# Performance work log

Measured on AMD Instinct MI355X. Metric: run time of the kernel, lower is better.

The kernel has to match this reference:

```python
import jax, jax.numpy as jnp
import numpy as np

H = 1024        # hidden_size
E = 8           # num_experts
K = 2           # top_k
FF = 4 * H      # expert hidden dim
B, S = 2, 2048


def setup_inputs() -> dict:
    key = jax.random.key(0)
    ks = jax.random.split(key, 7)
    scale = 0.02
    x = jax.random.normal(ks[0], (B, S, H), dtype=jnp.float32)
    Wg = jax.random.normal(ks[1], (H, E), dtype=jnp.float32) * scale
    bg = jnp.zeros((E,), dtype=jnp.float32)
    W1 = jax.random.normal(ks[2], (E, H, FF), dtype=jnp.float32) * scale
    b1 = jnp.zeros((E, FF), dtype=jnp.float32)
    W2 = jax.random.normal(ks[3], (E, FF, H), dtype=jnp.float32) * scale
    b2 = jnp.zeros((E, H), dtype=jnp.float32)
    return {"x": x, "Wg": Wg, "bg": bg, "W1": W1, "b1": b1, "W2": W2, "b2": b2}


def reference(x, Wg, bg, W1, b1, W2, b2):
    b, s, h = x.shape
    xf = x.reshape(-1, h)                                  # [T, H]
    T = xf.shape[0]
    # gating: softmax -> top-k -> renormalize
    probs = jax.nn.softmax(xf @ Wg + bg, axis=-1)          # [T, E]
    vals, idx = jax.lax.top_k(probs, K)                    # [T, K]
    vals = vals / jnp.sum(vals, axis=-1, keepdims=True)
    # dense combine weights: zero for non-selected experts (equivalent math)
    combine = jnp.zeros((T, E), dtype=x.dtype)
    combine = combine.at[jnp.arange(T)[:, None], idx].set(vals)  # [T, E]
    # all-expert FFN (GEMM-dominated), combined with sparse gate weights
    hmid = jax.nn.gelu(jnp.einsum('th,ehf->tef', xf, W1) + b1, approximate=False)  # [T,E,FF]
    y = jnp.einsum('tef,efh->teh', hmid, W2) + b2          # [T, E, H]
    out = jnp.einsum('te,teh->th', combine, y)             # [T, H]
    return out.reshape(b, s, h)
```

## Files before the change

kernel.cpp:

```cpp
#include <hip/hip_runtime.h>
#include <hip/hip_bf16.h>
#include <math.h>

#define T_TOK  4096
#define H_DIM  1024
#define E_NUM  8
#define FF_DIM 4096
#define KSEL   2
#define SLOTS  (T_TOK*KSEL)
#define SLOTS_PAD (SLOTS + 256)
#define BM 128
#define MAXTILES 72

typedef __attribute__((ext_vector_type(8))) short s16x8;
typedef __attribute__((ext_vector_type(8))) unsigned short u16x8;
typedef __attribute__((ext_vector_type(4))) float f32x4;

typedef __attribute__((address_space(1))) const void global_cvoid;
typedef __attribute__((address_space(3))) void lds_void;

__device__ __forceinline__ unsigned short f2bf(float f){
  unsigned int u = __float_as_uint(f);
  u += 0x7fffu + ((u>>16)&1u);
  return (unsigned short)(u>>16);
}
__device__ __forceinline__ float bf2f(unsigned short h){
  return __uint_as_float(((unsigned int)h)<<16);
}

static constexpr size_t OFF_CNT   = 0;
static constexpr size_t OFF_OFFS  = 256;
static constexpr size_t OFF_NT    = 512;
static constexpr size_t OFF_TILES = 768;
static constexpr size_t OFF_IDX   = 1280;
static constexpr size_t OFF_POS   = OFF_IDX  + 32768;
static constexpr size_t OFF_WV    = OFF_POS  + 32768;
static constexpr size_t OFF_SLOT  = OFF_WV   + 32768;
static constexpr size_t OFF_TOK   = OFF_SLOT + 32768;
static constexpr size_t OFF_WOF   = OFF_TOK  + 32768;
static constexpr size_t OFF_XG    = OFF_WOF  + 32768;
static constexpr size_t OFF_W1T   = OFF_XG  + (size_t)SLOTS_PAD*H_DIM*2;
static constexpr size_t OFF_W2T   = OFF_W1T + (size_t)E_NUM*H_DIM*FF_DIM*2;
static constexpr size_t OFF_MID   = OFF_W2T + (size_t)E_NUM*H_DIM*FF_DIM*2;
static constexpr size_t OFF_Y     = OFF_MID + (size_t)SLOTS_PAD*FF_DIM*2;

__global__ __launch_bounds__(64) void gate_kernel(
    const float* __restrict__ x, const float* __restrict__ Wg,
    const float* __restrict__ bg, int* __restrict__ cnt,
    int* __restrict__ idxp, int* __restrict__ posp, float* __restrict__ wvp)
{
  int t = blockIdx.x, lane = threadIdx.x;
  const float* xr = x + (size_t)t*H_DIM;
  float acc[E_NUM];
  #pragma unroll
  for (int e=0;e<E_NUM;e++) acc[e]=0.f;
  for (int i=0;i<H_DIM/64;i++){
    int h = i*64 + lane;
    float xv = xr[h];
    const float* wr_ = Wg + (size_t)h*E_NUM;
    #pragma unroll
    for (int e=0;e<E_NUM;e++) acc[e] += xv*wr_[e];
  }
  #pragma unroll
  for (int e=0;e<E_NUM;e++){
    #pragma unroll
    for (int off=32; off>0; off>>=1) acc[e] += __shfl_xor(acc[e], off);
  }
  if (lane==0){
    float l[E_NUM];
    #pragma unroll
    for (int e=0;e<E_NUM;e++) l[e] = acc[e] + bg[e];
    int i0 = 0;
    #pragma unroll
    for (int e=1;e<E_NUM;e++) if (l[e] > l[i0]) i0 = e;
    int i1 = (i0==0)?1:0;
    #pragma unroll
    for (int e=0;e<E_NUM;e++) if (e!=i0 && l[e] > l[i1]) i1 = e;
    float p1 = expf(l[i1]-l[i0]);
    float s  = 1.f + p1;
    float w0 = 1.f/s, w1 = p1/s;
    int pos0 = atomicAdd(&cnt[i0],1);
    int pos1 = atomicAdd(&cnt[i1],1);
    idxp[t*2]=i0; idxp[t*2+1]=i1;
    posp[t*2]=pos0; posp[t*2+1]=pos1;
    wvp[t*2]=w0; wvp[t*2+1]=w1;
  }
}

__global__ void plan_kernel(const int* __restrict__ cnt, int* __restrict__ offs,
                            int* __restrict__ tiles, int* __restrict__ ntiles)
{
  int o=0, n=0;
  for (int e=0;e<E_NUM;e++){
    offs[e]=o;
    int c=cnt[e];
    int nt=(c+BM-1)/BM;
    for (int m=0;m<nt;m++) tiles[n++] = (e<<16)|m;
    o+=c;
  }
  offs[E_NUM]=o;
  *ntiles=n;
}

__global__ void scatter_kernel(const int* __restrict__ idxp, const int* __restrict__ posp,
                               const float* __restrict__ wvp, const int* __restrict__ offs,
                               int* __restrict__ tok_of, float* __restrict__ w_of,
                               int* __restrict__ slot_of)
{
  int i = blockIdx.x*blockDim.x + threadIdx.x;
  if (i >= SLOTS) return;
  int t = i>>1, k = i&1;
  int e = idxp[t*2+k];
  int slot = offs[e] + posp[t*2+k];
  tok_of[slot] = t;
  w_of[slot]   = wvp[t*2+k];
  slot_of[t*2+k] = slot;
}

__global__ __launch_bounds__(256) void gather_kernel(
    const float* __restrict__ x, const int* __restrict__ tok_of,
    unsigned short* __restrict__ Xg)
{
  int slot = blockIdx.x;
  int t = tok_of[slot];
  const float4* src = (const float4*)(x + (size_t)t*H_DIM);
  float4 v = src[threadIdx.x];
  ushort4 o;
  o.x=f2bf(v.x); o.y=f2bf(v.y); o.z=f2bf(v.z); o.w=f2bf(v.w);
  ((ushort4*)(Xg + (size_t)slot*H_DIM))[threadIdx.x] = o;
}

__global__ __launch_bounds__(256) void transconv_kernel(
    const float* __restrict__ in, unsigned short* __restrict__ out, int R, int C)
{
  __shared__ float tile[64][65];
  int e = blockIdx.z;
  const float* inp = in + (size_t)e*R*C;
  unsigned short* op = out + (size_t)e*R*C;
  int c0 = blockIdx.x*64, r0 = blockIdx.y*64;
  int tx = threadIdx.x & 15, ty = threadIdx.x >> 4;
  #pragma unroll
  for (int i=0;i<4;i++){
    int r = i*16 + ty;
    float4 v = *(const float4*)(inp + (size_t)(r0+r)*C + c0 + tx*4);
    tile[r][tx*4+0]=v.x; tile[r][tx*4+1]=v.y; tile[r][tx*4+2]=v.z; tile[r][tx*4+3]=v.w;
  }
  __syncthreads();
  int wx = threadIdx.x & 7;
  int wcl = threadIdx.x >> 3;
  #pragma unroll
  for (int i=0;i<2;i++){
    int c = i*32 + wcl;
    u16x8 o;
    #pragma unroll
    for (int j=0;j<8;j++) o[j] = f2bf(tile[wx*8+j][c]);
    *(u16x8*)(op + (size_t)(c0+c)*R + r0 + wx*8) = o;
  }
}

#define GLDS(g, l) __builtin_amdgcn_global_load_lds((global_cvoid*)(g), (lds_void*)(l), 16, 0, 0)

template<int MODE>
__global__ __launch_bounds__(256, 4) void gemm128_kernel(
    const unsigned short* __restrict__ A,
    const unsigned short* __restrict__ Bt,
    const float* __restrict__ bias,
    unsigned short* __restrict__ Out,
    const int* __restrict__ tiles, const int* __restrict__ ntiles,
    const int* __restrict__ cnt, const int* __restrict__ offs,
    const float* __restrict__ w_of,
    int N, int K, int cshift)
{
  int tile_id = blockIdx.x >> cshift;
  if (tile_id >= *ntiles) return;
  int col0 = (blockIdx.x & ((1<<cshift)-1)) << 7;
  int packed = tiles[tile_id];
  int e = packed>>16, mt = packed & 0xffff;
  int row0 = offs[e] + mt*BM;
  int nvalid = cnt[e] - mt*BM; if (nvalid > BM) nvalid = BM;
  const unsigned short* Be = Bt + (size_t)e*N*K;

  __shared__ unsigned short As[2][128*32];
  __shared__ unsigned short Bs[2][128*32];
  char* asb = (char*)&As[0][0];
  char* bsb = (char*)&Bs[0][0];

  int t = threadIdx.x;
  int wid = t>>6, lane = t&63;
  int wr = (wid>>1)*64, wc = (wid&1)*64;
  int fr = lane&15, fq = lane>>4;

  int srow = t>>2;
  int sclog = ((t&3) - ((t>>3)&3)) & 3;
  int sdst = wid*1024;

  const unsigned short* gA0 = A  + (size_t)(row0 + srow)*K      + sclog*8;
  const unsigned short* gA1 = A  + (size_t)(row0 + 64 + srow)*K + sclog*8;
  const unsigned short* gB0 = Be + (size_t)(col0 + srow)*K      + sclog*8;
  const unsigned short* gB1 = Be + (size_t)(col0 + 64 + srow)*K + sclog*8;

  auto stage = [&](int buf, int kelem){
    GLDS(gA0 + kelem, asb + buf*8192 + sdst);
    GLDS(gA1 + kelem, asb + buf*8192 + 4096 + sdst);
    GLDS(gB0 + kelem, bsb + buf*8192 + sdst);
    GLDS(gB1 + kelem, bsb + buf*8192 + 4096 + sdst);
  };

  int rd_sw = ((fq + ((fr>>1)&3)) & 3) << 4;

  f32x4 acc[4][4];
  #pragma unroll
  for (int i=0;i<4;i++)
    #pragma unroll
    for (int j=0;j<4;j++) acc[i][j] = (f32x4){0.f,0.f,0.f,0.f};

  int NT = K >> 5;
  stage(0, 0);
  stage(1, 32);
  for (int kt=0; kt<NT; ++kt){
    int cur = kt&1;
    if (kt+1 < NT) asm volatile("s_waitcnt vmcnt(4)" ::: "memory");
    else           asm volatile("s_waitcnt vmcnt(0)" ::: "memory");
    __builtin_amdgcn_s_barrier();
    asm volatile("" ::: "memory");

    s16x8 af[4], bfr[4];
    #pragma unroll
    for (int i=0;i<4;i++){
      af[i]  = *(const s16x8*)(asb + cur*8192 + (wr + i*16 + fr)*64 + rd_sw);
      bfr[i] = *(const s16x8*)(bsb + cur*8192 + (wc + i*16 + fr)*64 + rd_sw);
    }
    #pragma unroll
    for (int i=0;i<4;i++)
      #pragma unroll
      for (int j=0;j<4;j++)
        acc[i][j] = __builtin_amdgcn_mfma_f32_16x16x32_bf16(af[i], bfr[j], acc[i][j], 0,0,0);

    asm volatile("s_waitcnt lgkmcnt(0)" ::: "memory");
    __builtin_amdgcn_s_barrier();
    asm volatile("" ::: "memory");
    if (kt+2 < NT) stage(cur, (kt+2)*32);
  }

  #pragma unroll
  for (int i=0;i<4;i++){
    #pragma unroll
    for (int r=0;r<4;r++){
      int lrow = wr + i*16 + fq*4 + r;
      if (lrow < nvalid){
        int grow = row0 + lrow;
        float scale = (MODE==1) ? w_of[grow] : 0.f;
        #pragma unroll
        for (int j=0;j<4;j++){
          int col = col0 + wc + j*16 + fr;
          float v = acc[i][j][r] + bias[(size_t)e*N + col];
          if (MODE==0) v = 0.5f*v*(1.f + erff(v*0.70710678118654752f));
          else         v *= scale;
          Out[(size_t)grow*N + col] = f2bf(v);
        }
      }
    }
  }
}

__global__ __launch_bounds__(256) void combine_kernel(
    const unsigned short* __restrict__ y, const int* __restrict__ slot_of,
    float* __restrict__ out)
{
  int tok = blockIdx.x;
  int s0 = slot_of[tok*2], s1 = slot_of[tok*2+1];
  const ushort4* y0 = (const ushort4*)(y + (size_t)s0*H_DIM);
  const ushort4* y1 = (const ushort4*)(y + (size_t)s1*H_DIM);
  float4* o = (float4*)(out + (size_t)tok*H_DIM);
  ushort4 a = y0[threadIdx.x], b = y1[threadIdx.x];
  float4 r;
  r.x = bf2f(a.x)+bf2f(b.x);
  r.y = bf2f(a.y)+bf2f(b.y);
  r.z = bf2f(a.z)+bf2f(b.z);
  r.w = bf2f(a.w)+bf2f(b.w);
  o[threadIdx.x] = r;
}

extern "C" void kernel_launch(void* const* d_in, const int* in_sizes, int n_in,
                              void* d_out, int out_size, void* d_ws, size_t ws_size,
                              hipStream_t stream) {
  const float* x  = (const float*)d_in[0];
  const float* Wg = (const float*)d_in[1];
  const float* bg = (const float*)d_in[2];
  const float* W1 = (const float*)d_in[3];
  const float* b1 = (const float*)d_in[4];
  const float* W2 = (const float*)d_in[5];
  const float* b2 = (const float*)d_in[6];
  float* out = (float*)d_out;
  char* ws = (char*)d_ws;

  int*   cnt      = (int*)  (ws + OFF_CNT);
  int*   offs     = (int*)  (ws + OFF_OFFS);
  int*   ntiles   = (int*)  (ws + OFF_NT);
  int*   tiles    = (int*)  (ws + OFF_TILES);
  int*   idxp     = (int*)  (ws + OFF_IDX);
  int*   posp     = (int*)  (ws + OFF_POS);
  float* wvp      = (float*)(ws + OFF_WV);
  int*   slot_of  = (int*)  (ws + OFF_SLOT);
  int*   tok_of   = (int*)  (ws + OFF_TOK);
  float* w_of     = (float*)(ws + OFF_WOF);
  unsigned short* Xg  = (unsigned short*)(ws + OFF_XG);
  unsigned short* W1t = (unsigned short*)(ws + OFF_W1T);
  unsigned short* W2t = (unsigned short*)(ws + OFF_W2T);
  unsigned short* mid = (unsigned short*)(ws + OFF_MID);
  unsigned short* y   = (unsigned short*)(ws + OFF_Y);

  hipMemsetAsync(ws + OFF_CNT, 0, 32, stream);

  gate_kernel<<<T_TOK, 64, 0, stream>>>(x, Wg, bg, cnt, idxp, posp, wvp);
  plan_kernel<<<1, 1, 0, stream>>>(cnt, offs, tiles, ntiles);
  scatter_kernel<<<SLOTS/256, 256, 0, stream>>>(idxp, posp, wvp, offs, tok_of, w_of, slot_of);
  gather_kernel<<<SLOTS, 256, 0, stream>>>(x, tok_of, Xg);

  transconv_kernel<<<dim3(FF_DIM/64, H_DIM/64, E_NUM), 256, 0, stream>>>(W1, W1t, H_DIM, FF_DIM);
  transconv_kernel<<<dim3(H_DIM/64, FF_DIM/64, E_NUM), 256, 0, stream>>>(W2, W2t, FF_DIM, H_DIM);

  gemm128_kernel<0><<<dim3(MAXTILES*32), 256, 0, stream>>>(
      Xg, W1t, b1, mid, tiles, ntiles, cnt, offs, nullptr, FF_DIM, H_DIM, 5);
  gemm128_kernel<1><<<dim3(MAXTILES*8), 256, 0, stream>>>(
      mid, W2t, b2, y, tiles, ntiles, cnt, offs, w_of, H_DIM, FF_DIM, 3);

  combine_kernel<<<T_TOK, 256, 0, stream>>>(y, slot_of, out);
}
```

Before: 463.5 us.

## Use 2-wave GEMM tiles and fuse combine into second GEMM via atomics

Rewrites the expert GEMM to run 128-thread blocks where each of two waves computes a 64x128 slice, so each wave does more MFMAs per B-fragment load. The second GEMM now scales by the gate weight and atomically adds fp32 results straight into the output, which removes the bf16 y buffer and the separate combine kernel. The output is zeroed with a memset. The gate kernel also handles four tokens per block. Risks are fewer waves to hide latency, higher register pressure from the 4x8 accumulators, and contention from the fp32 atomics.

```diff
diff --git a/kernel.cpp b/kernel.cpp
--- a/kernel.cpp
+++ b/kernel.cpp
@@ -35,55 +35,56 @@
 static constexpr size_t OFF_IDX   = 1280;
 static constexpr size_t OFF_POS   = OFF_IDX  + 32768;
 static constexpr size_t OFF_WV    = OFF_POS  + 32768;
-static constexpr size_t OFF_SLOT  = OFF_WV   + 32768;
-static constexpr size_t OFF_TOK   = OFF_SLOT + 32768;
+static constexpr size_t OFF_TOK   = OFF_WV   + 32768;
 static constexpr size_t OFF_WOF   = OFF_TOK  + 32768;
 static constexpr size_t OFF_XG    = OFF_WOF  + 32768;
 static constexpr size_t OFF_W1T   = OFF_XG  + (size_t)SLOTS_PAD*H_DIM*2;
 static constexpr size_t OFF_W2T   = OFF_W1T + (size_t)E_NUM*H_DIM*FF_DIM*2;
 static constexpr size_t OFF_MID   = OFF_W2T + (size_t)E_NUM*H_DIM*FF_DIM*2;
-static constexpr size_t OFF_Y     = OFF_MID + (size_t)SLOTS_PAD*FF_DIM*2;
 
 __global__ __launch_bounds__(64) void gate_kernel(
     const float* __restrict__ x, const float* __restrict__ Wg,
     const float* __restrict__ bg, int* __restrict__ cnt,
     int* __restrict__ idxp, int* __restrict__ posp, float* __restrict__ wvp)
 {
-  int t = blockIdx.x, lane = threadIdx.x;
-  const float* xr = x + (size_t)t*H_DIM;
-  float acc[E_NUM];
-  #pragma unroll
-  for (int e=0;e<E_NUM;e++) acc[e]=0.f;
-  for (int i=0;i<H_DIM/64;i++){
-    int h = i*64 + lane;
-    float xv = xr[h];
-    const float* wr_ = Wg + (size_t)h*E_NUM;
-    #pragma unroll
-    for (int e=0;e<E_NUM;e++) acc[e] += xv*wr_[e];
-  }
-  #pragma unroll
-  for (int e=0;e<E_NUM;e++){
-    #pragma unroll
-    for (int off=32; off>0; off>>=1) acc[e] += __shfl_xor(acc[e], off);
-  }
-  if (lane==0){
-    float l[E_NUM];
-    #pragma unroll
-    for (int e=0;e<E_NUM;e++) l[e] = acc[e] + bg[e];
-    int i0 = 0;
-    #pragma unroll
-    for (int e=1;e<E_NUM;e++) if (l[e] > l[i0]) i0 = e;
-    int i1 = (i0==0)?1:0;
-    #pragma unroll
-    for (int e=0;e<E_NUM;e++) if (e!=i0 && l[e] > l[i1]) i1 = e;
-    float p1 = expf(l[i1]-l[i0]);
-    float s  = 1.f + p1;
-    float w0 = 1.f/s, w1 = p1/s;
-    int pos0 = atomicAdd(&cnt[i0],1);
-    int pos1 = atomicAdd(&cnt[i1],1);
-    idxp[t*2]=i0; idxp[t*2+1]=i1;
-    posp[t*2]=pos0; posp[t*2+1]=pos1;
-    wvp[t*2]=w0; wvp[t*2+1]=w1;
+  int lane = threadIdx.x;
+  for (int tt=0; tt<4; ++tt){
+    int t = blockIdx.x*4 + tt;
+    const float* xr = x + (size_t)t*H_DIM;
+    float acc[E_NUM];
+    #pragma unroll
+    for (int e=0;e<E_NUM;e++) acc[e]=0.f;
+    for (int i=0;i<H_DIM/64;i++){
+      int h = i*64 + lane;
+      float xv = xr[h];
+      const float* wr_ = Wg + (size_t)h*E_NUM;
+      #pragma unroll
+      for (int e=0;e<E_NUM;e++) acc[e] += xv*wr_[e];
+    }
+    #pragma unroll
+    for (int e=0;e<E_NUM;e++){
+      #pragma unroll
+      for (int off=32; off>0; off>>=1) acc[e] += __shfl_xor(acc[e], off);
+    }
+    if (lane==0){
+      float l[E_NUM];
+      #pragma unroll
+      for (int e=0;e<E_NUM;e++) l[e] = acc[e] + bg[e];
+      int i0 = 0;
+      #pragma unroll
+      for (int e=1;e<E_NUM;e++) if (l[e] > l[i0]) i0 = e;
+      int i1 = (i0==0)?1:0;
+      #pragma unroll
+      for (int e=0;e<E_NUM;e++) if (e!=i0 && l[e] > l[i1]) i1 = e;
+      float p1 = expf(l[i1]-l[i0]);
+      float s  = 1.f + p1;
+      float w0 = 1.f/s, w1 = p1/s;
+      int pos0 = atomicAdd(&cnt[i0],1);
+      int pos1 = atomicAdd(&cnt[i1],1);
+      idxp[t*2]=i0; idxp[t*2+1]=i1;
+      posp[t*2]=pos0; posp[t*2+1]=pos1;
+      wvp[t*2]=w0; wvp[t*2+1]=w1;
+    }
   }
 }
 
@@ -104,8 +105,7 @@
 
 __global__ void scatter_kernel(const int* __restrict__ idxp, const int* __restrict__ posp,
                                const float* __restrict__ wvp, const int* __restrict__ offs,
-                               int* __restrict__ tok_of, float* __restrict__ w_of,
-                               int* __restrict__ slot_of)
+                               int* __restrict__ tok_of, float* __restrict__ w_of)
 {
   int i = blockIdx.x*blockDim.x + threadIdx.x;
   if (i >= SLOTS) return;
@@ -114,7 +114,6 @@
   int slot = offs[e] + posp[t*2+k];
   tok_of[slot] = t;
   w_of[slot]   = wvp[t*2+k];
-  slot_of[t*2+k] = slot;
 }
 
 __global__ __launch_bounds__(256) void gather_kernel(
@@ -161,11 +160,13 @@
 #define GLDS(g, l) __builtin_amdgcn_global_load_lds((global_cvoid*)(g), (lds_void*)(l), 16, 0, 0)
 
 template<int MODE>
-__global__ __launch_bounds__(256, 4) void gemm128_kernel(
+__global__ __launch_bounds__(128, 2) void gemm128w2_kernel(
     const unsigned short* __restrict__ A,
     const unsigned short* __restrict__ Bt,
     const float* __restrict__ bias,
     unsigned short* __restrict__ Out,
+    float* __restrict__ OutF,
+    const int* __restrict__ tok_of,
     const int* __restrict__ tiles, const int* __restrict__ ntiles,
     const int* __restrict__ cnt, const int* __restrict__ offs,
     const float* __restrict__ w_of,
@@ -180,61 +181,56 @@
   int nvalid = cnt[e] - mt*BM; if (nvalid > BM) nvalid = BM;
   const unsigned short* Be = Bt + (size_t)e*N*K;
 
-  __shared__ unsigned short As[2][128*32];
-  __shared__ unsigned short Bs[2][128*32];
-  char* asb = (char*)&As[0][0];
-  char* bsb = (char*)&Bs[0][0];
+  __shared__ char asb[2*8192];
+  __shared__ char bsb[2*8192];
 
   int t = threadIdx.x;
-  int wid = t>>6, lane = t&63;
-  int wr = (wid>>1)*64, wc = (wid&1)*64;
+  int w = t>>6, lane = t&63;
   int fr = lane&15, fq = lane>>4;
 
-  int srow = t>>2;
-  int sclog = ((t&3) - ((t>>3)&3)) & 3;
-  int sdst = wid*1024;
-
-  const unsigned short* gA0 = A  + (size_t)(row0 + srow)*K      + sclog*8;
-  const unsigned short* gA1 = A  + (size_t)(row0 + 64 + srow)*K + sclog*8;
-  const unsigned short* gB0 = Be + (size_t)(col0 + srow)*K      + sclog*8;
-  const unsigned short* gB1 = Be + (size_t)(col0 + 64 + srow)*K + sclog*8;
+  int srow = lane>>2;
+  int scl  = ((lane&3) - ((lane>>3)&3)) & 3;
+  const unsigned short* pA = A  + (size_t)(row0 + w*64 + srow)*K + scl*8;
+  const unsigned short* pB = Be + (size_t)(col0 + w*64 + srow)*K + scl*8;
 
   auto stage = [&](int buf, int kelem){
-    GLDS(gA0 + kelem, asb + buf*8192 + sdst);
-    GLDS(gA1 + kelem, asb + buf*8192 + 4096 + sdst);
-    GLDS(gB0 + kelem, bsb + buf*8192 + sdst);
-    GLDS(gB1 + kelem, bsb + buf*8192 + 4096 + sdst);
+    #pragma unroll
+    for (int i=0;i<4;i++){
+      GLDS(pA + (size_t)i*16*K + kelem, asb + buf*8192 + w*4096 + i*1024);
+      GLDS(pB + (size_t)i*16*K + kelem, bsb + buf*8192 + w*4096 + i*1024);
+    }
   };
 
-  int rd_sw = ((fq + ((fr>>1)&3)) & 3) << 4;
-
-  f32x4 acc[4][4];
+  int rdc = ((fq + ((fr>>1)&3)) & 3) << 4;
+
+  f32x4 acc[4][8];
   #pragma unroll
-  for (int i=0;i<4;i++)
-    #pragma unroll
-    for (int j=0;j<4;j++) acc[i][j] = (f32x4){0.f,0.f,0.f,0.f};
+  for (int m=0;m<4;m++)
+    #pragma unroll
+    for (int n=0;n<8;n++) acc[m][n] = (f32x4){0.f,0.f,0.f,0.f};
 
   int NT = K >> 5;
   stage(0, 0);
   stage(1, 32);
   for (int kt=0; kt<NT; ++kt){
     int cur = kt&1;
-    if (kt+1 < NT) asm volatile("s_waitcnt vmcnt(4)" ::: "memory");
+    if (kt+1 < NT) asm volatile("s_waitcnt vmcnt(8)" ::: "memory");
     else           asm volatile("s_waitcnt vmcnt(0)" ::: "memory");
     __builtin_amdgcn_s_barrier();
     asm volatile("" ::: "memory");
 
-    s16x8 af[4], bfr[4];
-    #pragma unroll
-    for (int i=0;i<4;i++){
-      af[i]  = *(const s16x8*)(asb + cur*8192 + (wr + i*16 + fr)*64 + rd_sw);
-      bfr[i] = *(const s16x8*)(bsb + cur*8192 + (wc + i*16 + fr)*64 + rd_sw);
-    }
-    #pragma unroll
-    for (int i=0;i<4;i++)
-      #pragma unroll
-      for (int j=0;j<4;j++)
-        acc[i][j] = __builtin_amdgcn_mfma_f32_16x16x32_bf16(af[i], bfr[j], acc[i][j], 0,0,0);
+    s16x8 af[4], bfr[8];
+    #pragma unroll
+    for (int m=0;m<4;m++)
+      af[m] = *(const s16x8*)(asb + cur*8192 + (w*64 + m*16 + fr)*64 + rdc);
+    #pragma unroll
+    for (int n=0;n<8;n++)
+      bfr[n] = *(const s16x8*)(bsb + cur*8192 + (n*16 + fr)*64 + rdc);
+    #pragma unroll
+    for (int m=0;m<4;m++)
+      #pragma unroll
+      for (int n=0;n<8;n++)
+        acc[m][n] = __builtin_amdgcn_mfma_f32_16x16x32_bf16(af[m], bfr[n], acc[m][n], 0,0,0);
 
     asm volatile("s_waitcnt lgkmcnt(0)" ::: "memory");
     __builtin_amdgcn_s_barrier();
@@ -243,42 +239,33 @@
   }
 
   #pragma unroll
-  for (int i=0;i<4;i++){
+  for (int m=0;m<4;m++){
     #pragma unroll
     for (int r=0;r<4;r++){
-      int lrow = wr + i*16 + fq*4 + r;
+      int lrow = w*64 + m*16 + fq*4 + r;
       if (lrow < nvalid){
         int grow = row0 + lrow;
-        float scale = (MODE==1) ? w_of[grow] : 0.f;
-        #pragma unroll
-        for (int j=0;j<4;j++){
-          int col = col0 + wc + j*16 + fr;
-          float v = acc[i][j][r] + bias[(size_t)e*N + col];
-          if (MODE==0) v = 0.5f*v*(1.f + erff(v*0.70710678118654752f));
-          else         v *= scale;
-          Out[(size_t)grow*N + col] = f2bf(v);
+        if (MODE==0){
+          #pragma unroll
+          for (int n=0;n<8;n++){
+            int col = col0 + n*16 + fr;
+            float v = acc[m][n][r] + bias[(size_t)e*N + col];
+            v = 0.5f*v*(1.f + erff(v*0.70710678118654752f));
+            Out[(size_t)grow*N + col] = f2bf(v);
+          }
+        } else {
+          int tok = tok_of[grow];
+          float scale = w_of[grow];
+          #pragma unroll
+          for (int n=0;n<8;n++){
+            int col = col0 + n*16 + fr;
+            float v = (acc[m][n][r] + bias[(size_t)e*N + col]) * scale;
+            atomicAdd(&OutF[(size_t)tok*H_DIM + col], v);
+          }
         }
       }
     }
   }
-}
-
-__global__ __launch_bounds__(256) void combine_kernel(
-    const unsigned short* __restrict__ y, const int* __restrict__ slot_of,
-    float* __restrict__ out)
-{
-  int tok = blockIdx.x;
-  int s0 = slot_of[tok*2], s1 = slot_of[tok*2+1];
-  const ushort4* y0 = (const ushort4*)(y + (size_t)s0*H_DIM);
-  const ushort4* y1 = (const ushort4*)(y + (size_t)s1*H_DIM);
-  float4* o = (float4*)(out + (size_t)tok*H_DIM);
-  ushort4 a = y0[threadIdx.x], b = y1[threadIdx.x];
-  float4 r;
-  r.x = bf2f(a.x)+bf2f(b.x);
-  r.y = bf2f(a.y)+bf2f(b.y);
-  r.z = bf2f(a.z)+bf2f(b.z);
-  r.w = bf2f(a.w)+bf2f(b.w);
-  o[threadIdx.x] = r;
 }
 
 extern "C" void kernel_launch(void* const* d_in, const int* in_sizes, int n_in,
@@ -301,29 +288,28 @@
   int*   idxp     = (int*)  (ws + OFF_IDX);
   int*   posp     = (int*)  (ws + OFF_POS);
   float* wvp      = (float*)(ws + OFF_WV);
-  int*   slot_of  = (int*)  (ws + OFF_SLOT);
   int*   tok_of   = (int*)  (ws + OFF_TOK);
   float* w_of     = (float*)(ws + OFF_WOF);
   unsigned short* Xg  = (unsigned short*)(ws + OFF_XG);
   unsigned short* W1t = (unsigned short*)(ws + OFF_W1T);
   unsigned short* W2t = (unsigned short*)(ws + OFF_W2T);
   unsigned short* mid = (unsigned short*)(ws + OFF_MID);
-  unsigned short* y   = (unsigned short*)(ws + OFF_Y);
 
   hipMemsetAsync(ws + OFF_CNT, 0, 32, stream);
-
-  gate_kernel<<<T_TOK, 64, 0, stream>>>(x, Wg, bg, cnt, idxp, posp, wvp);
+  hipMemsetAsync(d_out, 0, (size_t)out_size*sizeof(float), stream);
+
+  gate_kernel<<<T_TOK/4, 64, 0, stream>>>(x, Wg, bg, cnt, idxp, posp, wvp);
   plan_kernel<<<1, 1, 0, stream>>>(cnt, offs, tiles, ntiles);
-  scatter_kernel<<<SLOTS/256, 256, 0, stream>>>(idxp, posp, wvp, offs, tok_of, w_of, slot_of);
+  scatter_kernel<<<SLOTS/256, 256, 0, stream>>>(idxp, posp, wvp, offs, tok_of, w_of);
   gather_kernel<<<SLOTS, 256, 0, stream>>>(x, tok_of, Xg);
 
   transconv_kernel<<<dim3(FF_DIM/64, H_DIM/64, E_NUM), 256, 0, stream>>>(W1, W1t, H_DIM, FF_DIM);
   transconv_kernel<<<dim3(H_DIM/64, FF_DIM/64, E_NUM), 256, 0, stream>>>(W2, W2t, FF_DIM, H_DIM);
 
-  gemm128_kernel<0><<<dim3(MAXTILES*32), 256, 0, stream>>>(
-      Xg, W1t, b1, mid, tiles, ntiles, cnt, offs, nullptr, FF_DIM, H_DIM, 5);
-  gemm128_kernel<1><<<dim3(MAXTILES*8), 256, 0, stream>>>(
-      mid, W2t, b2, y, tiles, ntiles, cnt, offs, w_of, H_DIM, FF_DIM, 3);
-
-  combine_kernel<<<T_TOK, 256, 0, stream>>>(y, slot_of, out);
-}
+  gemm128w2_kernel<0><<<dim3(MAXTILES*32), 128, 0, stream>>>(
+      Xg, W1t, b1, mid, nullptr, tok_of, tiles, ntiles, cnt, offs, nullptr,
+      FF_DIM, H_DIM, 5);
+  gemm128w2_kernel<1><<<dim3(MAXTILES*8), 128, 0, stream>>>(
+      mid, W2t, b2, nullptr, out, tok_of, tiles, ntiles, cnt, offs, w_of,
+      H_DIM, FF_DIM, 3);
+}
```

Result: slower. 571.0 us (+23.2%).

## Use 256x256 tiled GEMM for first expert FFN layer with new tile plan

Applied to the files above, without the earlier changes.

Adds a 512-thread gemm256s kernel with 256x256 output tiles, K-step 64, XOR-swizzled LDS and double buffering for the first expert GEMM. The plan kernel now also builds a 256-row tile list, so each block reuses more of A and B per load. The gate kernel now processes four tokens per block to cut launch count. The bigger tiles waste more work on padded rows per expert, and occupancy falls to two blocks of 128 KB LDS each.

```diff
diff --git a/kernel.cpp b/kernel.cpp
--- a/kernel.cpp
+++ b/kernel.cpp
@@ -11,6 +11,7 @@
 #define SLOTS_PAD (SLOTS + 256)
 #define BM 128
 #define MAXTILES 72
+#define MAXT256  40
 
 typedef __attribute__((ext_vector_type(8))) short s16x8;
 typedef __attribute__((ext_vector_type(8))) unsigned short u16x8;
@@ -31,7 +32,9 @@
 static constexpr size_t OFF_CNT   = 0;
 static constexpr size_t OFF_OFFS  = 256;
 static constexpr size_t OFF_NT    = 512;
+static constexpr size_t OFF_NT256 = 516;
 static constexpr size_t OFF_TILES = 768;
+static constexpr size_t OFF_T256  = 1088;
 static constexpr size_t OFF_IDX   = 1280;
 static constexpr size_t OFF_POS   = OFF_IDX  + 32768;
 static constexpr size_t OFF_WV    = OFF_POS  + 32768;
@@ -49,57 +52,64 @@
     const float* __restrict__ bg, int* __restrict__ cnt,
     int* __restrict__ idxp, int* __restrict__ posp, float* __restrict__ wvp)
 {
-  int t = blockIdx.x, lane = threadIdx.x;
-  const float* xr = x + (size_t)t*H_DIM;
-  float acc[E_NUM];
-  #pragma unroll
-  for (int e=0;e<E_NUM;e++) acc[e]=0.f;
-  for (int i=0;i<H_DIM/64;i++){
-    int h = i*64 + lane;
-    float xv = xr[h];
-    const float* wr_ = Wg + (size_t)h*E_NUM;
-    #pragma unroll
-    for (int e=0;e<E_NUM;e++) acc[e] += xv*wr_[e];
-  }
-  #pragma unroll
-  for (int e=0;e<E_NUM;e++){
-    #pragma unroll
-    for (int off=32; off>0; off>>=1) acc[e] += __shfl_xor(acc[e], off);
-  }
-  if (lane==0){
-    float l[E_NUM];
-    #pragma unroll
-    for (int e=0;e<E_NUM;e++) l[e] = acc[e] + bg[e];
-    int i0 = 0;
-    #pragma unroll
-    for (int e=1;e<E_NUM;e++) if (l[e] > l[i0]) i0 = e;
-    int i1 = (i0==0)?1:0;
-    #pragma unroll
-    for (int e=0;e<E_NUM;e++) if (e!=i0 && l[e] > l[i1]) i1 = e;
-    float p1 = expf(l[i1]-l[i0]);
-    float s  = 1.f + p1;
-    float w0 = 1.f/s, w1 = p1/s;
-    int pos0 = atomicAdd(&cnt[i0],1);
-    int pos1 = atomicAdd(&cnt[i1],1);
-    idxp[t*2]=i0; idxp[t*2+1]=i1;
-    posp[t*2]=pos0; posp[t*2+1]=pos1;
-    wvp[t*2]=w0; wvp[t*2+1]=w1;
+  int lane = threadIdx.x;
+  for (int tt=0; tt<4; ++tt){
+    int t = blockIdx.x*4 + tt;
+    const float* xr = x + (size_t)t*H_DIM;
+    float acc[E_NUM];
+    #pragma unroll
+    for (int e=0;e<E_NUM;e++) acc[e]=0.f;
+    for (int i=0;i<H_DIM/64;i++){
+      int h = i*64 + lane;
+      float xv = xr[h];
+      const float* wr_ = Wg + (size_t)h*E_NUM;
+      #pragma unroll
+      for (int e=0;e<E_NUM;e++) acc[e] += xv*wr_[e];
+    }
+    #pragma unroll
+    for (int e=0;e<E_NUM;e++){
+      #pragma unroll
+      for (int off=32; off>0; off>>=1) acc[e] += __shfl_xor(acc[e], off);
+    }
+    if (lane==0){
+      float l[E_NUM];
+      #pragma unroll
+      for (int e=0;e<E_NUM;e++) l[e] = acc[e] + bg[e];
+      int i0 = 0;
+      #pragma unroll
+      for (int e=1;e<E_NUM;e++) if (l[e] > l[i0]) i0 = e;
+      int i1 = (i0==0)?1:0;
+      #pragma unroll
+      for (int e=0;e<E_NUM;e++) if (e!=i0 && l[e] > l[i1]) i1 = e;
+      float p1 = expf(l[i1]-l[i0]);
+      float s  = 1.f + p1;
+      float w0 = 1.f/s, w1 = p1/s;
+      int pos0 = atomicAdd(&cnt[i0],1);
+      int pos1 = atomicAdd(&cnt[i1],1);
+      idxp[t*2]=i0; idxp[t*2+1]=i1;
+      posp[t*2]=pos0; posp[t*2+1]=pos1;
+      wvp[t*2]=w0; wvp[t*2+1]=w1;
+    }
   }
 }
 
 __global__ void plan_kernel(const int* __restrict__ cnt, int* __restrict__ offs,
-                            int* __restrict__ tiles, int* __restrict__ ntiles)
-{
-  int o=0, n=0;
+                            int* __restrict__ tiles, int* __restrict__ ntiles,
+                            int* __restrict__ tiles256, int* __restrict__ ntiles256)
+{
+  int o=0, n=0, n2=0;
   for (int e=0;e<E_NUM;e++){
     offs[e]=o;
     int c=cnt[e];
     int nt=(c+BM-1)/BM;
     for (int m=0;m<nt;m++) tiles[n++] = (e<<16)|m;
+    int nt2=(c+255)/256;
+    for (int m=0;m<nt2;m++) tiles256[n2++] = (e<<16)|m;
     o+=c;
   }
   offs[E_NUM]=o;
   *ntiles=n;
+  *ntiles256=n2;
 }
 
 __global__ void scatter_kernel(const int* __restrict__ idxp, const int* __restrict__ posp,
@@ -160,7 +170,112 @@
 
 #define GLDS(g, l) __builtin_amdgcn_global_load_lds((global_cvoid*)(g), (lds_void*)(l), 16, 0, 0)
 
-template<int MODE>
+__global__ __launch_bounds__(512, 2) void gemm256s_kernel(
+    const unsigned short* __restrict__ A,
+    const unsigned short* __restrict__ Bt,
+    const float* __restrict__ bias,
+    unsigned short* __restrict__ Out,
+    const int* __restrict__ tiles256, const int* __restrict__ ntiles256,
+    const int* __restrict__ cnt, const int* __restrict__ offs,
+    int N, int K)
+{
+  int tile_id = blockIdx.x >> 4;
+  if (tile_id >= *ntiles256) return;
+  int col0 = (blockIdx.x & 15) << 8;
+  int packed = tiles256[tile_id];
+  int e = packed>>16, mt = packed & 0xffff;
+  int row0 = offs[e] + mt*256;
+  int nvalid = cnt[e] - mt*256; if (nvalid > 256) nvalid = 256;
+  const unsigned short* Be = Bt + (size_t)e*N*K;
+
+  __shared__ char asb[2*32768];
+  __shared__ char bsb[2*32768];
+
+  int t = threadIdx.x;
+  int wid = t>>6, lane = t&63;
+  int wm = wid>>2, wn = wid&3;
+  int fr = lane&15, fq = lane>>4;
+
+  int lr  = t>>3;
+  int lch = (t&7) ^ (lr&7);
+  int wbase = wid*1024;
+  const unsigned short* pA = A  + (size_t)(row0 + lr)*K + lch*8;
+  const unsigned short* pB = Be + (size_t)(col0 + lr)*K + lch*8;
+
+  auto stageAll = [&](int buf, int kt){
+    int ke = kt*64;
+    #pragma unroll
+    for (int j=0;j<4;j++)
+      GLDS(pA + (size_t)j*64*K + ke, asb + buf*32768 + j*8192 + wbase);
+    #pragma unroll
+    for (int j=0;j<4;j++)
+      GLDS(pB + (size_t)j*64*K + ke, bsb + buf*32768 + j*8192 + wbase);
+  };
+
+  #define RD_A(buf,m,ks) (*(const s16x8*)(asb + (buf)*32768 + (wm*128+(m)*16+fr)*128 + ((((ks)*4+fq) ^ (fr&7))<<4)))
+  #define RD_B(buf,n,ks) (*(const s16x8*)(bsb + (buf)*32768 + (wn*64 +(n)*16+fr)*128 + ((((ks)*4+fq) ^ (fr&7))<<4)))
+
+  f32x4 acc[8][4];
+  #pragma unroll
+  for (int i=0;i<8;i++)
+    #pragma unroll
+    for (int j=0;j<4;j++) acc[i][j] = (f32x4){0.f,0.f,0.f,0.f};
+
+  int NT = K >> 6;
+  stageAll(0, 0);
+  asm volatile("s_waitcnt vmcnt(0)" ::: "memory");
+  __builtin_amdgcn_s_barrier();
+  asm volatile("" ::: "memory");
+
+  for (int kt=0; kt<NT; ++kt){
+    int cur = kt&1;
+    if (kt+1 < NT) stageAll(cur^1, kt+1);
+
+    #pragma unroll
+    for (int ks=0; ks<2; ++ks){
+      s16x8 af[8], bf[4];
+      #pragma unroll
+      for (int m=0;m<8;m++) af[m] = RD_A(cur, m, ks);
+      #pragma unroll
+      for (int n=0;n<4;n++) bf[n] = RD_B(cur, n, ks);
+      __builtin_amdgcn_s_setprio(1);
+      #pragma unroll
+      for (int m=0;m<8;m++)
+        #pragma unroll
+        for (int n=0;n<4;n++)
+          acc[m][n] = __builtin_amdgcn_mfma_f32_16x16x32_bf16(af[m], bf[n], acc[m][n], 0,0,0);
+      __builtin_amdgcn_s_setprio(0);
+    }
+
+    asm volatile("s_waitcnt vmcnt(0)" ::: "memory");
+    __builtin_amdgcn_s_barrier();
+    asm volatile("" ::: "memory");
+  }
+
+  float bias_v[4];
+  #pragma unroll
+  for (int n=0;n<4;n++) bias_v[n] = bias[(size_t)e*N + col0 + wn*64 + n*16 + fr];
+  #pragma unroll
+  for (int m=0;m<8;m++){
+    #pragma unroll
+    for (int r=0;r<4;r++){
+      int lrow = wm*128 + m*16 + fq*4 + r;
+      if (lrow < nvalid){
+        int grow = row0 + lrow;
+        #pragma unroll
+        for (int n=0;n<4;n++){
+          int col = col0 + wn*64 + n*16 + fr;
+          float v = acc[m][n][r] + bias_v[n];
+          v = 0.5f*v*(1.f + erff(v*0.70710678118654752f));
+          Out[(size_t)grow*N + col] = f2bf(v);
+        }
+      }
+    }
+  }
+  #undef RD_A
+  #undef RD_B
+}
+
 __global__ __launch_bounds__(256, 4) void gemm128_kernel(
     const unsigned short* __restrict__ A,
     const unsigned short* __restrict__ Bt,
@@ -191,19 +306,19 @@
   int fr = lane&15, fq = lane>>4;
 
   int srow = t>>2;
-  int sclog = ((t&3) - ((t>>3)&3)) & 3;
+  int scl  = ((t&3) - ((t>>3)&3)) & 3;
   int sdst = wid*1024;
 
-  const unsigned short* gA0 = A  + (size_t)(row0 + srow)*K      + sclog*8;
-  const unsigned short* gA1 = A  + (size_t)(row0 + 64 + srow)*K + sclog*8;
-  const unsigned short* gB0 = Be + (size_t)(col0 + srow)*K      + sclog*8;
-  const unsigned short* gB1 = Be + (size_t)(col0 + 64 + srow)*K + sclog*8;
+  const unsigned short* pA0 = A  + (size_t)(row0 + srow)*K      + scl*8;
+  const unsigned short* pA1 = A  + (size_t)(row0 + 64 + srow)*K + scl*8;
+  const unsigned short* pB0 = Be + (size_t)(col0 + srow)*K      + scl*8;
+  const unsigned short* pB1 = Be + (size_t)(col0 + 64 + srow)*K + scl*8;
 
   auto stage = [&](int buf, int kelem){
-    GLDS(gA0 + kelem, asb + buf*8192 + sdst);
-    GLDS(gA1 + kelem, asb + buf*8192 + 4096 + sdst);
-    GLDS(gB0 + kelem, bsb + buf*8192 + sdst);
-    GLDS(gB1 + kelem, bsb + buf*8192 + 4096 + sdst);
+    GLDS(pA0 + kelem, asb + buf*8192 + sdst);
+    GLDS(pA1 + kelem, asb + buf*8192 + 4096 + sdst);
+    GLDS(pB0 + kelem, bsb + buf*8192 + sdst);
+    GLDS(pB1 + kelem, bsb + buf*8192 + 4096 + sdst);
   };
 
   int rd_sw = ((fq + ((fr>>1)&3)) & 3) << 4;
@@ -249,13 +364,11 @@
       int lrow = wr + i*16 + fq*4 + r;
       if (lrow < nvalid){
         int grow = row0 + lrow;
-        float scale = (MODE==1) ? w_of[grow] : 0.f;
+        float scale = w_of[grow];
         #pragma unroll
         for (int j=0;j<4;j++){
           int col = col0 + wc + j*16 + fr;
-          float v = acc[i][j][r] + bias[(size_t)e*N + col];
-          if (MODE==0) v = 0.5f*v*(1.f + erff(v*0.70710678118654752f));
-          else         v *= scale;
+          float v = (acc[i][j][r] + bias[(size_t)e*N + col]) * scale;
           Out[(size_t)grow*N + col] = f2bf(v);
         }
       }
@@ -297,7 +410,9 @@
   int*   cnt      = (int*)  (ws + OFF_CNT);
   int*   offs     = (int*)  (ws + OFF_OFFS);
   int*   ntiles   = (int*)  (ws + OFF_NT);
+  int*   ntiles256= (int*)  (ws + OFF_NT256);
   int*   tiles    = (int*)  (ws + OFF_TILES);
+  int*   tiles256 = (int*)  (ws + OFF_T256);
   int*   idxp     = (int*)  (ws + OFF_IDX);
   int*   posp     = (int*)  (ws + OFF_POS);
   float* wvp      = (float*)(ws + OFF_WV);
@@ -312,17 +427,17 @@
 
   hipMemsetAsync(ws + OFF_CNT, 0, 32, stream);
 
-  gate_kernel<<<T_TOK, 64, 0, stream>>>(x, Wg, bg, cnt, idxp, posp, wvp);
-  plan_kernel<<<1, 1, 0, stream>>>(cnt, offs, tiles, ntiles);
+  gate_kernel<<<T_TOK/4, 64, 0, stream>>>(x, Wg, bg, cnt, idxp, posp, wvp);
+  plan_kernel<<<1, 1, 0, stream>>>(cnt, offs, tiles, ntiles, tiles256, ntiles256);
   scatter_kernel<<<SLOTS/256, 256, 0, stream>>>(idxp, posp, wvp, offs, tok_of, w_of, slot_of);
   gather_kernel<<<SLOTS, 256, 0, stream>>>(x, tok_of, Xg);
 
   transconv_kernel<<<dim3(FF_DIM/64, H_DIM/64, E_NUM), 256, 0, stream>>>(W1, W1t, H_DIM, FF_DIM);
   transconv_kernel<<<dim3(H_DIM/64, FF_DIM/64, E_NUM), 256, 0, stream>>>(W2, W2t, FF_DIM, H_DIM);
 
-  gemm128_kernel<0><<<dim3(MAXTILES*32), 256, 0, stream>>>(
-      Xg, W1t, b1, mid, tiles, ntiles, cnt, offs, nullptr, FF_DIM, H_DIM, 5);
-  gemm128_kernel<1><<<dim3(MAXTILES*8), 256, 0, stream>>>(
+  gemm256s_kernel<<<dim3(MAXT256*16), 512, 0, stream>>>(
+      Xg, W1t, b1, mid, tiles256, ntiles256, cnt, offs, FF_DIM, H_DIM);
+  gemm128_kernel<<<dim3(MAXTILES*8), 256, 0, stream>>>(
       mid, W2t, b2, y, tiles, ntiles, cnt, offs, w_of, H_DIM, FF_DIM, 3);
 
   combine_kernel<<<T_TOK, 256, 0, stream>>>(y, slot_of, out);
```

Result: slower. 495.1 us (+6.8%).
